# Kernel optimization log

Hardware: AMD Instinct MI355X
Metric: run time of the kernel (lower is better)

Reference implementation:

```python
import jax, jax.numpy as jnp
import numpy as np


def setup_inputs() -> dict:
    key = jax.random.key(0)
    k_u, k_lam, k_B, k_C = jax.random.split(key, 4)
    batch, seq_len, d_model, N = 4, 4096, 1024, 64
    return {
        "u": jax.random.normal(k_u, (batch, seq_len, d_model), dtype=jnp.float32),
        "Lambda": jax.random.normal(k_lam, (N,), dtype=jnp.float32),
        "log_dt": jnp.zeros((1,), dtype=jnp.float32),
        "B": jax.random.normal(k_B, (N, d_model), dtype=jnp.float32),
        "C": jax.random.normal(k_C, (d_model, N), dtype=jnp.float32),
        "D": jnp.zeros((d_model,), dtype=jnp.float32),
    }


def reference(u, Lambda, log_dt, B, C, D):
    # dt = exp(log_dt); A = diag(exp(dt * (-exp(Lambda)))) -> diagonal decay vector a of shape (N,)
    dt = jnp.exp(log_dt)          # (1,)
    a = jnp.exp(-dt * jnp.exp(Lambda))  # (N,)

    # Precompute input projection for all timesteps: Bu[b, t, n] = u[b, t] @ B.T
    Bu = jnp.einsum("bld,nd->bln", u, B)  # (batch, L, N)

    # Sequential diagonal recurrence: x_t = a * x_{t-1} + Bu_t
    def step(x, bu_t):
        x = a * x + bu_t
        return x, x

    x0 = jnp.zeros((u.shape[0], Lambda.shape[0]), dtype=u.dtype)
    _, xs = jax.lax.scan(step, x0, jnp.swapaxes(Bu, 0, 1))  # xs: (L, batch, N)
    xs = jnp.swapaxes(xs, 0, 1)  # (batch, L, N)

    # Output projection + skip: y_t = x_t @ C.T + D * u_t
    return jnp.einsum("bln,dn->bld", xs, C) + D * u
```

## Files before the change

kernel.cpp:

```cpp
#include <hip/hip_runtime.h>


constexpr int BATCH  = 4;
constexpr int L      = 4096;
constexpr int DM     = 1024;
constexpr int N      = 64;
constexpr int ROWS   = BATCH * L;
constexpr int CHUNK  = 64;
constexpr int NCHUNK = L / CHUNK;

typedef __attribute__((ext_vector_type(8))) short     bf16x8;
typedef __attribute__((ext_vector_type(4))) float     f32x4;

__device__ __forceinline__ unsigned short f2bf(float f) {
  unsigned int u = __float_as_uint(f);
  u += 0x7FFFu + ((u >> 16) & 1u);
  return (unsigned short)(u >> 16);
}

__global__ __launch_bounds__(256) void bu_scan(const float* __restrict__ u,
                                               const float* __restrict__ Bm,
                                               const float* __restrict__ Lambda,
                                               const float* __restrict__ log_dt,
                                               float* __restrict__ xs,
                                               float* __restrict__ F) {
  __shared__ __align__(16) char smem[36864];
  typedef unsigned short AsT[64][72];
  AsT* As = reinterpret_cast<AsT*>(smem);
  AsT* Bs = reinterpret_cast<AsT*>(smem + 18432);
  float (*T)[68] = reinterpret_cast<float (*)[68]>(smem);

  const int tid  = threadIdx.x;
  const int lane = tid & 63;
  const int wv   = tid >> 6;
  const int l15  = lane & 15;
  const int g    = lane >> 4;
  const int row0 = blockIdx.x * 64;

  const int sr = tid >> 4;
  const int sq = tid & 15;

  f32x4 acc[4] = {};
  float4 pa[4], pb[4];

  constexpr int NCH = DM / 64;
  #pragma unroll
  for (int i = 0; i < 4; ++i) {
    const int r = sr + i * 16;
    pa[i] = *reinterpret_cast<const float4*>(&u[(long)(row0 + r) * DM + sq * 4]);
    pb[i] = *reinterpret_cast<const float4*>(&Bm[(long)r * DM + sq * 4]);
  }

  for (int c = 0; c < NCH; ++c) {
    const int buf = c & 1;
    if (c) __syncthreads();
    #pragma unroll
    for (int i = 0; i < 4; ++i) {
      const int r = sr + i * 16;
      ushort4 ha = make_ushort4(f2bf(pa[i].x), f2bf(pa[i].y), f2bf(pa[i].z), f2bf(pa[i].w));
      ushort4 hb = make_ushort4(f2bf(pb[i].x), f2bf(pb[i].y), f2bf(pb[i].z), f2bf(pb[i].w));
      *reinterpret_cast<ushort4*>(&As[buf][r][sq * 4]) = ha;
      *reinterpret_cast<ushort4*>(&Bs[buf][r][sq * 4]) = hb;
    }
    __syncthreads();
    if (c + 1 < NCH) {
      const int kb = (c + 1) * 64;
      #pragma unroll
      for (int i = 0; i < 4; ++i) {
        const int r = sr + i * 16;
        pa[i] = *reinterpret_cast<const float4*>(&u[(long)(row0 + r) * DM + kb + sq * 4]);
        pb[i] = *reinterpret_cast<const float4*>(&Bm[(long)r * DM + kb + sq * 4]);
      }
    }
    #pragma unroll
    for (int ks = 0; ks < 2; ++ks) {
      const bf16x8 af = *reinterpret_cast<const bf16x8*>(
          &As[buf][wv * 16 + l15][ks * 32 + g * 8]);
      #pragma unroll
      for (int t = 0; t < 4; ++t) {
        const bf16x8 bfr = *reinterpret_cast<const bf16x8*>(
            &Bs[buf][t * 16 + l15][ks * 32 + g * 8]);
        acc[t] = __builtin_amdgcn_mfma_f32_16x16x32_bf16(af, bfr, acc[t], 0, 0, 0);
      }
    }
  }

  __syncthreads();
  #pragma unroll
  for (int t = 0; t < 4; ++t)
    #pragma unroll
    for (int r = 0; r < 4; ++r)
      T[wv * 16 + g * 4 + r][t * 16 + l15] = acc[t][r];
  __syncthreads();

  if (tid < 64) {
    const int n = tid;
    const float dt = __expf(log_dt[0]);
    const float a  = __expf(-dt * __expf(Lambda[n]));
    float v[CHUNK];
    #pragma unroll
    for (int s = 0; s < CHUNK; ++s) v[s] = T[s][n];
    const long base = (long)row0 * N + n;
    float x = 0.0f;
    #pragma unroll
    for (int s = 0; s < CHUNK; ++s) {
      x = fmaf(a, x, v[s]);
      xs[base + s * N] = x;
    }
    F[blockIdx.x * N + n] = x;
  }
}

__global__ __launch_bounds__(256) void carry_scan(const float* __restrict__ F,
                                                  const float* __restrict__ Lambda,
                                                  const float* __restrict__ log_dt,
                                                  float* __restrict__ carry) {
  const int t = threadIdx.x;
  const int b = t >> 6;
  const int n = t & 63;
  const float dt = __expf(log_dt[0]);
  const float w  = -dt * __expf(Lambda[n]);
  const float aS = __expf(w * (float)CHUNK);

  float f[NCHUNK];
  #pragma unroll
  for (int c = 0; c < NCHUNK; ++c) f[c] = F[(b * NCHUNK + c) * N + n];

  float P = 0.0f;
  #pragma unroll
  for (int c = 0; c < NCHUNK; ++c) {
    carry[(b * NCHUNK + c) * N + n] = P;
    P = fmaf(aS, P, f[c]);
  }
}

__global__ __launch_bounds__(256) void y_gemm(const float* __restrict__ xs,
                                              const float* __restrict__ carry,
                                              const float* __restrict__ Lambda,
                                              const float* __restrict__ log_dt,
                                              const float* __restrict__ Cm,
                                              const float* __restrict__ Dv,
                                              const float* __restrict__ u,
                                              float* __restrict__ y) {
  __shared__ __align__(16) char smem[33792];
  unsigned short (*Xs)[72] = reinterpret_cast<unsigned short (*)[72]>(smem);
  unsigned short (*Cs)[72] = reinterpret_cast<unsigned short (*)[72]>(smem + 9216);
  float (*T)[132] = reinterpret_cast<float (*)[132]>(smem);
  __shared__ float wS[64], ciS[64], Dsh[128];

  const int tid  = threadIdx.x;
  const int lane = tid & 63;
  const int wv   = tid >> 6;
  const int l15  = lane & 15;
  const int g    = lane >> 4;
  const int row0 = (blockIdx.x & 255) * 64;
  const int d0   = (blockIdx.x >> 8) * 128;

  if (tid < 64) {
    const float dt = __expf(log_dt[0]);
    wS[tid]  = -dt * __expf(Lambda[tid]);
    ciS[tid] = carry[row0 + tid];
  }
  if (tid < 128) Dsh[tid] = Dv[d0 + tid];
  __syncthreads();

  #pragma unroll
  for (int i = 0; i < 4; ++i) {
    const int idx = tid + i * 256;
    const int r = idx >> 4, q = idx & 15;
    float4 v = *reinterpret_cast<const float4*>(&xs[(long)(row0 + r) * N + q * 4]);
    const float p = (float)(r + 1);
    v.x += __expf(wS[q * 4 + 0] * p) * ciS[q * 4 + 0];
    v.y += __expf(wS[q * 4 + 1] * p) * ciS[q * 4 + 1];
    v.z += __expf(wS[q * 4 + 2] * p) * ciS[q * 4 + 2];
    v.w += __expf(wS[q * 4 + 3] * p) * ciS[q * 4 + 3];
    *reinterpret_cast<ushort4*>(&Xs[r][q * 4]) =
        make_ushort4(f2bf(v.x), f2bf(v.y), f2bf(v.z), f2bf(v.w));
  }
  #pragma unroll
  for (int i = 0; i < 8; ++i) {
    const int idx = tid + i * 256;
    const int r = idx >> 4, q = idx & 15;
    const float4 v = *reinterpret_cast<const float4*>(&Cm[(long)(d0 + r) * N + q * 4]);
    *reinterpret_cast<ushort4*>(&Cs[r][q * 4]) =
        make_ushort4(f2bf(v.x), f2bf(v.y), f2bf(v.z), f2bf(v.w));
  }
  __syncthreads();

  bf16x8 af[2];
  #pragma unroll
  for (int ks = 0; ks < 2; ++ks)
    af[ks] = *reinterpret_cast<const bf16x8*>(&Xs[wv * 16 + l15][ks * 32 + g * 8]);

  f32x4 acc[8] = {};
  #pragma unroll
  for (int t = 0; t < 8; ++t) {
    #pragma unroll
    for (int ks = 0; ks < 2; ++ks) {
      const bf16x8 bfr = *reinterpret_cast<const bf16x8*>(
          &Cs[t * 16 + l15][ks * 32 + g * 8]);
      acc[t] = __builtin_amdgcn_mfma_f32_16x16x32_bf16(af[ks], bfr, acc[t], 0, 0, 0);
    }
  }

  __syncthreads();
  #pragma unroll
  for (int t = 0; t < 8; ++t)
    #pragma unroll
    for (int r = 0; r < 4; ++r)
      T[wv * 16 + g * 4 + r][t * 16 + l15] = acc[t][r];
  __syncthreads();

  #pragma unroll
  for (int i = 0; i < 8; ++i) {
    const int id = tid + i * 256;
    const int r = id >> 5;
    const int q = id & 31;
    float4 v = *reinterpret_cast<const float4*>(&T[r][q * 4]);
    const float4 dd = *reinterpret_cast<const float4*>(&Dsh[q * 4]);
    if (dd.x != 0.0f || dd.y != 0.0f || dd.z != 0.0f || dd.w != 0.0f) {
      const float4 uu = *reinterpret_cast<const float4*>(
          &u[(long)(row0 + r) * DM + d0 + q * 4]);
      v.x = fmaf(dd.x, uu.x, v.x);
      v.y = fmaf(dd.y, uu.y, v.y);
      v.z = fmaf(dd.z, uu.z, v.z);
      v.w = fmaf(dd.w, uu.w, v.w);
    }
    *reinterpret_cast<float4*>(&y[(long)(row0 + r) * DM + d0 + q * 4]) = v;
  }
}

extern "C" void kernel_launch(void* const* d_in, const int* in_sizes, int n_in,
                              void* d_out, int out_size, void* d_ws, size_t ws_size,
                              hipStream_t stream) {
  const float* u      = (const float*)d_in[0];
  const float* Lambda = (const float*)d_in[1];
  const float* log_dt = (const float*)d_in[2];
  const float* Bm     = (const float*)d_in[3];
  const float* Cm     = (const float*)d_in[4];
  const float* Dv     = (const float*)d_in[5];
  float* y = (float*)d_out;

  const size_t planeB = (size_t)ROWS * N;
  float* xs    = (float*)d_ws;
  float* F     = xs + planeB;
  float* carry = F + (size_t)BATCH * NCHUNK * N;

  bu_scan<<<ROWS / 64, 256, 0, stream>>>(u, Bm, Lambda, log_dt, xs, F);
  carry_scan<<<1, 256, 0, stream>>>(F, Lambda, log_dt, carry);
  y_gemm<<<(ROWS / 64) * (DM / 128), 256, 0, stream>>>(xs, carry, Lambda, log_dt,
                                                       Cm, Dv, u, y);
}
```

Measured before the change: 38.54 us.

## Store xs in bf16, parallelize chunk scan across waves, precompute decay table

Several changes land together. The intermediate state xs is now written as bf16, which halves its global traffic between kernels. The in-block 64-step scan, previously run by a single wave, is split across all four waves with a small cross-wave carry fixup. The per-element exp decay in y_gemm is replaced by a decay table that carry_scan computes once. The u/B load prefetch is also deepened to two stages, and bf16 packing now uses the hardware float2-to-bf16 conversion. Storing xs in bf16 adds a little extra rounding before the carry is added.

Result: slower. 67.88 us (+76.1%).

```diff
diff --git a/kernel.cpp b/kernel.cpp
--- a/kernel.cpp
+++ b/kernel.cpp
@@ -1,4 +1,5 @@
 #include <hip/hip_runtime.h>
+#include <hip/hip_bf16.h>
 
 
 constexpr int BATCH  = 4;
@@ -12,23 +13,23 @@
 typedef __attribute__((ext_vector_type(8))) short     bf16x8;
 typedef __attribute__((ext_vector_type(4))) float     f32x4;
 
-__device__ __forceinline__ unsigned short f2bf(float f) {
-  unsigned int u = __float_as_uint(f);
-  u += 0x7FFFu + ((u >> 16) & 1u);
-  return (unsigned short)(u >> 16);
+__device__ __forceinline__ unsigned int pk2(float x, float y) {
+  __hip_bfloat162 h = __float22bfloat162_rn(make_float2(x, y));
+  return *reinterpret_cast<unsigned int*>(&h);
 }
 
 __global__ __launch_bounds__(256) void bu_scan(const float* __restrict__ u,
                                                const float* __restrict__ Bm,
                                                const float* __restrict__ Lambda,
                                                const float* __restrict__ log_dt,
-                                               float* __restrict__ xs,
+                                               unsigned short* __restrict__ xsb,
                                                float* __restrict__ F) {
   __shared__ __align__(16) char smem[36864];
-  typedef unsigned short AsT[64][72];
-  AsT* As = reinterpret_cast<AsT*>(smem);
-  AsT* Bs = reinterpret_cast<AsT*>(smem + 18432);
+  typedef unsigned short HalfT[64][72];
+  HalfT* As = reinterpret_cast<HalfT*>(smem);
+  HalfT* Bs = reinterpret_cast<HalfT*>(smem + 18432);
   float (*T)[68] = reinterpret_cast<float (*)[68]>(smem);
+  float* W = reinterpret_cast<float*>(smem + 17408);
 
   const int tid  = threadIdx.x;
   const int lane = tid & 63;
@@ -41,45 +42,49 @@
   const int sq = tid & 15;
 
   f32x4 acc[4] = {};
-  float4 pa[4], pb[4];
+  float4 pa[2][4], pb[2][4];
 
   constexpr int NCH = DM / 64;
   #pragma unroll
-  for (int i = 0; i < 4; ++i) {
-    const int r = sr + i * 16;
-    pa[i] = *reinterpret_cast<const float4*>(&u[(long)(row0 + r) * DM + sq * 4]);
-    pb[i] = *reinterpret_cast<const float4*>(&Bm[(long)r * DM + sq * 4]);
-  }
-
-  for (int c = 0; c < NCH; ++c) {
-    const int buf = c & 1;
-    if (c) __syncthreads();
+  for (int s = 0; s < 2; ++s) {
+    const int kb = s * 64;
     #pragma unroll
     for (int i = 0; i < 4; ++i) {
       const int r = sr + i * 16;
-      ushort4 ha = make_ushort4(f2bf(pa[i].x), f2bf(pa[i].y), f2bf(pa[i].z), f2bf(pa[i].w));
-      ushort4 hb = make_ushort4(f2bf(pb[i].x), f2bf(pb[i].y), f2bf(pb[i].z), f2bf(pb[i].w));
-      *reinterpret_cast<ushort4*>(&As[buf][r][sq * 4]) = ha;
-      *reinterpret_cast<ushort4*>(&Bs[buf][r][sq * 4]) = hb;
+      pa[s][i] = *reinterpret_cast<const float4*>(&u[(long)(row0 + r) * DM + kb + sq * 4]);
+      pb[s][i] = *reinterpret_cast<const float4*>(&Bm[(long)r * DM + kb + sq * 4]);
+    }
+  }
+
+  for (int c = 0; c < NCH; ++c) {
+    const int s = c & 1;
+    if (c) __syncthreads();
+    #pragma unroll
+    for (int i = 0; i < 4; ++i) {
+      const int r = sr + i * 16;
+      uint2 ha = {pk2(pa[s][i].x, pa[s][i].y), pk2(pa[s][i].z, pa[s][i].w)};
+      uint2 hb = {pk2(pb[s][i].x, pb[s][i].y), pk2(pb[s][i].z, pb[s][i].w)};
+      *reinterpret_cast<uint2*>(&As[s][r][sq * 4]) = ha;
+      *reinterpret_cast<uint2*>(&Bs[s][r][sq * 4]) = hb;
     }
     __syncthreads();
-    if (c + 1 < NCH) {
-      const int kb = (c + 1) * 64;
+    if (c + 2 < NCH) {
+      const int kb = (c + 2) * 64;
       #pragma unroll
       for (int i = 0; i < 4; ++i) {
         const int r = sr + i * 16;
-        pa[i] = *reinterpret_cast<const float4*>(&u[(long)(row0 + r) * DM + kb + sq * 4]);
-        pb[i] = *reinterpret_cast<const float4*>(&Bm[(long)r * DM + kb + sq * 4]);
+        pa[s][i] = *reinterpret_cast<const float4*>(&u[(long)(row0 + r) * DM + kb + sq * 4]);
+        pb[s][i] = *reinterpret_cast<const float4*>(&Bm[(long)r * DM + kb + sq * 4]);
       }
     }
     #pragma unroll
     for (int ks = 0; ks < 2; ++ks) {
       const bf16x8 af = *reinterpret_cast<const bf16x8*>(
-          &As[buf][wv * 16 + l15][ks * 32 + g * 8]);
+          &As[s][wv * 16 + l15][ks * 32 + g * 8]);
       #pragma unroll
       for (int t = 0; t < 4; ++t) {
         const bf16x8 bfr = *reinterpret_cast<const bf16x8*>(
-            &Bs[buf][t * 16 + l15][ks * 32 + g * 8]);
+            &Bs[s][t * 16 + l15][ks * 32 + g * 8]);
         acc[t] = __builtin_amdgcn_mfma_f32_16x16x32_bf16(af, bfr, acc[t], 0, 0, 0);
       }
     }
@@ -93,28 +98,45 @@
       T[wv * 16 + g * 4 + r][t * 16 + l15] = acc[t][r];
   __syncthreads();
 
-  if (tid < 64) {
-    const int n = tid;
-    const float dt = __expf(log_dt[0]);
-    const float a  = __expf(-dt * __expf(Lambda[n]));
-    float v[CHUNK];
-    #pragma unroll
-    for (int s = 0; s < CHUNK; ++s) v[s] = T[s][n];
-    const long base = (long)row0 * N + n;
+  const float dtv = __expf(log_dt[0]);
+  const float wn  = -dtv * __expf(Lambda[lane]);
+  const float a   = __expf(wn);
+  const float a16 = __expf(wn * 16.0f);
+
+  float p[16];
+  {
     float x = 0.0f;
     #pragma unroll
-    for (int s = 0; s < CHUNK; ++s) {
-      x = fmaf(a, x, v[s]);
-      xs[base + s * N] = x;
-    }
-    F[blockIdx.x * N + n] = x;
+    for (int j = 0; j < 16; ++j) { x = fmaf(a, x, T[wv * 16 + j][lane]); p[j] = x; }
+    W[wv * 64 + lane] = x;
+  }
+  __syncthreads();
+  float P = 0.0f;
+  #pragma unroll
+  for (int w2 = 0; w2 < 3; ++w2)
+    if (w2 < wv) P = fmaf(a16, P, W[w2 * 64 + lane]);
+  __syncthreads();
+  float cfac = P;
+  #pragma unroll
+  for (int j = 0; j < 16; ++j) { cfac *= a; T[wv * 16 + j][lane] = p[j] + cfac; }
+  if (wv == 3) F[blockIdx.x * N + lane] = p[15] + cfac;
+  __syncthreads();
+
+  #pragma unroll
+  for (int i = 0; i < 4; ++i) {
+    const int idx = tid + i * 256;
+    const int r = idx >> 4, q = idx & 15;
+    const float4 v = *reinterpret_cast<const float4*>(&T[r][q * 4]);
+    uint2 o = {pk2(v.x, v.y), pk2(v.z, v.w)};
+    *reinterpret_cast<uint2*>(&xsb[(long)(row0 + r) * N + q * 4]) = o;
   }
 }
 
 __global__ __launch_bounds__(256) void carry_scan(const float* __restrict__ F,
                                                   const float* __restrict__ Lambda,
                                                   const float* __restrict__ log_dt,
-                                                  float* __restrict__ carry) {
+                                                  float* __restrict__ carry,
+                                                  float* __restrict__ dec) {
   const int t = threadIdx.x;
   const int b = t >> 6;
   const int n = t & 63;
@@ -122,6 +144,12 @@
   const float w  = -dt * __expf(Lambda[n]);
   const float aS = __expf(w * (float)CHUNK);
 
+  #pragma unroll
+  for (int i = 0; i < 16; ++i) {
+    const int tt = b * 16 + i;
+    dec[tt * N + n] = __expf(w * (float)(tt + 1));
+  }
+
   float f[NCHUNK];
   #pragma unroll
   for (int c = 0; c < NCHUNK; ++c) f[c] = F[(b * NCHUNK + c) * N + n];
@@ -134,10 +162,9 @@
   }
 }
 
-__global__ __launch_bounds__(256) void y_gemm(const float* __restrict__ xs,
+__global__ __launch_bounds__(256) void y_gemm(const unsigned short* __restrict__ xsb,
                                               const float* __restrict__ carry,
-                                              const float* __restrict__ Lambda,
-                                              const float* __restrict__ log_dt,
+                                              const float* __restrict__ dec,
                                               const float* __restrict__ Cm,
                                               const float* __restrict__ Dv,
                                               const float* __restrict__ u,
@@ -146,7 +173,7 @@
   unsigned short (*Xs)[72] = reinterpret_cast<unsigned short (*)[72]>(smem);
   unsigned short (*Cs)[72] = reinterpret_cast<unsigned short (*)[72]>(smem + 9216);
   float (*T)[132] = reinterpret_cast<float (*)[132]>(smem);
-  __shared__ float wS[64], ciS[64], Dsh[128];
+  __shared__ float ciS[64], Dsh[128];
 
   const int tid  = threadIdx.x;
   const int lane = tid & 63;
@@ -156,34 +183,42 @@
   const int row0 = (blockIdx.x & 255) * 64;
   const int d0   = (blockIdx.x >> 8) * 128;
 
-  if (tid < 64) {
-    const float dt = __expf(log_dt[0]);
-    wS[tid]  = -dt * __expf(Lambda[tid]);
-    ciS[tid] = carry[row0 + tid];
-  }
+  if (tid < 64)  ciS[tid] = carry[row0 + tid];
   if (tid < 128) Dsh[tid] = Dv[d0 + tid];
   __syncthreads();
 
   #pragma unroll
-  for (int i = 0; i < 4; ++i) {
+  for (int i = 0; i < 2; ++i) {
     const int idx = tid + i * 256;
-    const int r = idx >> 4, q = idx & 15;
-    float4 v = *reinterpret_cast<const float4*>(&xs[(long)(row0 + r) * N + q * 4]);
-    const float p = (float)(r + 1);
-    v.x += __expf(wS[q * 4 + 0] * p) * ciS[q * 4 + 0];
-    v.y += __expf(wS[q * 4 + 1] * p) * ciS[q * 4 + 1];
-    v.z += __expf(wS[q * 4 + 2] * p) * ciS[q * 4 + 2];
-    v.w += __expf(wS[q * 4 + 3] * p) * ciS[q * 4 + 3];
-    *reinterpret_cast<ushort4*>(&Xs[r][q * 4]) =
-        make_ushort4(f2bf(v.x), f2bf(v.y), f2bf(v.z), f2bf(v.w));
+    const int r = idx >> 3, q = idx & 7;
+    const uint4 xv = *reinterpret_cast<const uint4*>(&xsb[(long)(row0 + r) * N + q * 8]);
+    const float4 dv0 = *reinterpret_cast<const float4*>(&dec[r * N + q * 8]);
+    const float4 dv1 = *reinterpret_cast<const float4*>(&dec[r * N + q * 8 + 4]);
+    float f[8];
+    #pragma unroll
+    for (int j = 0; j < 4; ++j) {
+      const unsigned int wbits = (&xv.x)[j];
+      f[2 * j]     = __uint_as_float(wbits << 16);
+      f[2 * j + 1] = __uint_as_float(wbits & 0xFFFF0000u);
+    }
+    f[0] = fmaf(dv0.x, ciS[q * 8 + 0], f[0]);
+    f[1] = fmaf(dv0.y, ciS[q * 8 + 1], f[1]);
+    f[2] = fmaf(dv0.z, ciS[q * 8 + 2], f[2]);
+    f[3] = fmaf(dv0.w, ciS[q * 8 + 3], f[3]);
+    f[4] = fmaf(dv1.x, ciS[q * 8 + 4], f[4]);
+    f[5] = fmaf(dv1.y, ciS[q * 8 + 5], f[5]);
+    f[6] = fmaf(dv1.z, ciS[q * 8 + 6], f[6]);
+    f[7] = fmaf(dv1.w, ciS[q * 8 + 7], f[7]);
+    uint4 o = {pk2(f[0], f[1]), pk2(f[2], f[3]), pk2(f[4], f[5]), pk2(f[6], f[7])};
+    *reinterpret_cast<uint4*>(&Xs[r][q * 8]) = o;
   }
   #pragma unroll
   for (int i = 0; i < 8; ++i) {
     const int idx = tid + i * 256;
     const int r = idx >> 4, q = idx & 15;
     const float4 v = *reinterpret_cast<const float4*>(&Cm[(long)(d0 + r) * N + q * 4]);
-    *reinterpret_cast<ushort4*>(&Cs[r][q * 4]) =
-        make_ushort4(f2bf(v.x), f2bf(v.y), f2bf(v.z), f2bf(v.w));
+    uint2 o = {pk2(v.x, v.y), pk2(v.z, v.w)};
+    *reinterpret_cast<uint2*>(&Cs[r][q * 4]) = o;
   }
   __syncthreads();
 
@@ -242,12 +277,12 @@
   float* y = (float*)d_out;
 
   const size_t planeB = (size_t)ROWS * N;
-  float* xs    = (float*)d_ws;
-  float* F     = xs + planeB;
+  unsigned short* xsb = (unsigned short*)d_ws;
+  float* F     = (float*)(xsb + planeB);
   float* carry = F + (size_t)BATCH * NCHUNK * N;
-
-  bu_scan<<<ROWS / 64, 256, 0, stream>>>(u, Bm, Lambda, log_dt, xs, F);
-  carry_scan<<<1, 256, 0, stream>>>(F, Lambda, log_dt, carry);
-  y_gemm<<<(ROWS / 64) * (DM / 128), 256, 0, stream>>>(xs, carry, Lambda, log_dt,
-                                                       Cm, Dv, u, y);
-}
+  float* dec   = carry + (size_t)BATCH * NCHUNK * N;
+
+  bu_scan<<<ROWS / 64, 256, 0, stream>>>(u, Bm, Lambda, log_dt, xsb, F);
+  carry_scan<<<1, 256, 0, stream>>>(F, Lambda, log_dt, carry, dec);
+  y_gemm<<<(ROWS / 64) * (DM / 128), 256, 0, stream>>>(xsb, carry, dec, Cm, Dv, u, y);
+}
```
